# Kernel optimization log

Hardware: AMD Instinct MI355X
Metric: run time of the kernel (lower is better)

The kernel has to match this reference:

```python
import jax, jax.numpy as jnp
import numpy as np

N_NODES = 50000
N_EDGES = 800000
N_GRAPHS = 256
F_IN, HID, EMB = 128, 256, 128
N_GROUPS, N_FAM = 16, 128


def setup_inputs() -> dict:
    key = jax.random.key(0)
    ks = jax.random.split(key, 12)
    x = jax.random.normal(ks[0], (N_NODES, F_IN), dtype=jnp.float32)
    edge_index = jax.random.randint(ks[1], (2, N_EDGES), 0, N_NODES, dtype=jnp.int64)
    batch = jnp.sort(jax.random.randint(ks[2], (N_NODES,), 0, N_GRAPHS, dtype=jnp.int64))
    def lin(k, fi, fo):
        s = 1.0 / np.sqrt(fi)
        return jax.random.uniform(k, (fi, fo), minval=-s, maxval=s, dtype=jnp.float32)
    W1 = lin(ks[3], F_IN, HID); b1 = jnp.zeros((HID,), jnp.float32)
    W2 = lin(ks[4], HID, EMB); b2 = jnp.zeros((EMB,), jnp.float32)
    Wg = lin(ks[5], EMB, N_GROUPS); bg = jnp.zeros((N_GROUPS,), jnp.float32)
    s = 1.0 / np.sqrt(EMB)
    Wf = jax.random.uniform(ks[6], (N_GROUPS, EMB, N_FAM), minval=-s, maxval=s, dtype=jnp.float32)
    bf = jnp.zeros((N_GROUPS, N_FAM), jnp.float32)
    return {"x": x, "edge_index": edge_index, "batch": batch,
            "W1": W1, "b1": b1, "W2": W2, "b2": b2,
            "Wg": Wg, "bg": bg, "Wf": Wf, "bf": bf}


def _gcn_conv(h, src, dst, coef, W, b, n):
    # h: [N, Fin]; src/dst: [E'] (self-loops included); coef: [E'] sym-norm
    hw = h @ W                                    # [N, Fout]
    msg = hw[src] * coef[:, None]                 # gather + scale, [E', Fout]
    out = jax.ops.segment_sum(msg, dst, num_segments=n)  # scatter-add
    return out + b


def reference(x, edge_index, batch, W1, b1, W2, b2, Wg, bg, Wf, bf):
    n = x.shape[0]
    loops = jnp.arange(n, dtype=edge_index.dtype)
    src = jnp.concatenate([edge_index[0], loops])
    dst = jnp.concatenate([edge_index[1], loops])
    # symmetric GCN normalization (deg >= 1 thanks to self-loops)
    deg = jax.ops.segment_sum(jnp.ones_like(dst, dtype=x.dtype), dst, num_segments=n)
    dinv = jax.lax.rsqrt(deg)
    coef = dinv[src] * dinv[dst]

    h1 = jax.nn.relu(_gcn_conv(x, src, dst, coef, W1, b1, n))  # dropout = identity (eval)
    h2 = _gcn_conv(h1, src, dst, coef, W2, b2, n)

    # global mean pool over graphs
    sums = jax.ops.segment_sum(h2, batch, num_segments=N_GRAPHS)
    cnts = jax.ops.segment_sum(jnp.ones((n,), x.dtype), batch, num_segments=N_GRAPHS)
    embeddings = sums / jnp.maximum(cnts, 1.0)[:, None]        # [G, EMB]

    group_logits = embeddings @ Wg + bg                        # [G, n_groups]
    pred_groups = jnp.argmax(group_logits, axis=1)             # routing
    # per-graph routed family classifier (dense equivalent of the dict outputs)
    family_logits = jnp.einsum('gd,gdf->gf', embeddings, Wf[pred_groups]) + bf[pred_groups]
    return embeddings, group_logits, family_logits
```

## Files before the change

kernel.cpp:

```cpp
#include <hip/hip_runtime.h>
#include <hip/hip_fp16.h>
#include <cstddef>
#include <cstdint>

static constexpr int NN   = 50000;
static constexpr int NE   = 800000;
static constexpr int NG   = 256;
static constexpr int FIN  = 128;
static constexpr int HID  = 256;
static constexpr int EMB  = 128;
static constexpr int NGRP = 16;
static constexpr int NFAM = 128;
static constexpr int NETOT = NE + NN;

static constexpr int SCAN_B  = 256;
static constexpr int SCAN_CH = (NN + SCAN_B - 1) / SCAN_B;

using bf16x8 = __attribute__((ext_vector_type(8))) short;
using f32x4  = __attribute__((ext_vector_type(4))) float;

__device__ __forceinline__ unsigned short f2bf(float f) {
    uint32_t u = __float_as_uint(f);
    u += 0x7FFFu + ((u >> 16) & 1u);
    return (unsigned short)(u >> 16);
}
__device__ __forceinline__ float bf2f(unsigned short u) {
    return __uint_as_float((uint32_t)u << 16);
}
__device__ __forceinline__ void unpack_sw(uint32_t v, int& s, float& w) {
    s = (int)(v & 0xFFFFu);
    w = __half2float(__ushort_as_half((unsigned short)(v >> 16)));
}


__global__ void k_count(const int* __restrict__ edst, int* __restrict__ degi, int e) {
    int i = blockIdx.x * blockDim.x + threadIdx.x;
    if (i < e) atomicAdd(degi + edst[i], 1);
}

__global__ void k_prep(const int* __restrict__ degi, const int* __restrict__ batch,
                       float* __restrict__ dinv, int* __restrict__ gstart,
                       float* __restrict__ emb_acc, int n, int G) {
    int i = blockIdx.x * blockDim.x + threadIdx.x;
    if (i < NG * EMB) emb_acc[i] = 0.f;
    if (i >= n) return;
    dinv[i] = rsqrtf((float)(degi[i] + 1));
    int b  = batch[i];
    int pb = (i == 0) ? -1 : batch[i - 1];
    for (int g = pb + 1; g <= b; ++g) gstart[g] = i;
    if (i == n - 1) {
        for (int g = b + 1; g <= G; ++g) gstart[g] = n;
    }
}

__global__ void k_xconv(const float* __restrict__ x, const float* __restrict__ dinv,
                        unsigned short* __restrict__ xs) {
    int t = blockIdx.x * blockDim.x + threadIdx.x;
    size_t i = (size_t)t * 8;
    float dv = dinv[t >> 4];
    float4 a = *(const float4*)(x + i);
    float4 b = *(const float4*)(x + i + 4);
    uint4 o;
    o.x = (uint32_t)f2bf(dv * a.x) | ((uint32_t)f2bf(dv * a.y) << 16);
    o.y = (uint32_t)f2bf(dv * a.z) | ((uint32_t)f2bf(dv * a.w) << 16);
    o.z = (uint32_t)f2bf(dv * b.x) | ((uint32_t)f2bf(dv * b.y) << 16);
    o.w = (uint32_t)f2bf(dv * b.z) | ((uint32_t)f2bf(dv * b.w) << 16);
    *(uint4*)(xs + i) = o;
}

__global__ void k_wconv(const float* __restrict__ W1, const float* __restrict__ W2,
                        unsigned short* __restrict__ W1t, unsigned short* __restrict__ W2t) {
    int t = blockIdx.x * blockDim.x + threadIdx.x;
    if (t < HID * FIN) {
        int nidx = t >> 7, k = t & 127;
        W1t[t] = f2bf(W1[(size_t)k * HID + nidx]);
    } else {
        int u = t - HID * FIN;
        int nidx = u >> 8, k = u & 255;
        W2t[u] = f2bf(W2[(size_t)k * EMB + nidx]);
    }
}


__global__ __launch_bounds__(256) void k_scanA(const int* __restrict__ degi,
                                               const int* __restrict__ gstart,
                                               float* __restrict__ rcnt,
                                               int* __restrict__ row_ptr,
                                               int* __restrict__ bsum, int n) {
    const int b = blockIdx.x, t = threadIdx.x;
    if (b == 0 && t < NG) {
        int c = gstart[t + 1] - gstart[t];
        rcnt[t] = 1.0f / (float)max(c, 1);
    }
    __shared__ int sh[256];
    const int idx = b * SCAN_CH + t;
    int v = 0;
    if (t < SCAN_CH && idx < n) v = degi[idx] + 1;
    sh[t] = v;
    __syncthreads();
    for (int off = 1; off < 256; off <<= 1) {
        int y = (t >= off) ? sh[t - off] : 0;
        __syncthreads();
        if (t >= off) sh[t] += y;
        __syncthreads();
    }
    if (t < SCAN_CH && idx < n) row_ptr[idx] = sh[t] - v;
    if (t == 255) bsum[b] = sh[255];
}

__global__ __launch_bounds__(256) void k_scanB(const int* __restrict__ bsum,
                                               const int* __restrict__ batch,
                                               const float* __restrict__ dinv,
                                               const float* __restrict__ rcnt,
                                               int* __restrict__ row_ptr,
                                               unsigned long long* __restrict__ combo,
                                               uint32_t* __restrict__ eP, int n) {
    __shared__ int sh[SCAN_B];
    const int b = blockIdx.x, t = threadIdx.x;
    sh[t] = bsum[t];
    __syncthreads();
    for (int off = 1; off < SCAN_B; off <<= 1) {
        int y = (t >= off) ? sh[t - off] : 0;
        __syncthreads();
        if (t >= off) sh[t] += y;
        __syncthreads();
    }
    const int boff = (b == 0) ? 0 : sh[b - 1];
    const int idx  = b * SCAN_CH + t;
    if (t < SCAN_CH && idx < n) {
        int rp = row_ptr[idx] + boff;
        row_ptr[idx] = rp;
        unsigned short wh = __half_as_ushort(
            __float2half(dinv[idx] * rcnt[batch[idx]]));
        combo[idx] = ((unsigned long long)wh << 32) | (unsigned int)(rp + 1);
        eP[rp] = (uint32_t)idx | ((uint32_t)wh << 16);
    }
    if (b == 0 && t == 0) row_ptr[n] = sh[SCAN_B - 1];
}


__global__ void k_build(const int* __restrict__ esrc, const int* __restrict__ edst,
                        unsigned long long* __restrict__ combo,
                        uint32_t* __restrict__ eP, int e) {
    int j = blockIdx.x * blockDim.x + threadIdx.x;
    if (j >= e) return;
    int d = edst[j];
    int s = esrc[j];
    unsigned long long old = atomicAdd(combo + d, 1ull);
    uint32_t slot = (uint32_t)old;
    uint32_t wh   = (uint32_t)(old >> 32) & 0xFFFFu;
    eP[slot] = (uint32_t)s | (wh << 16);
}


__global__ __launch_bounds__(256) void k_agg(
        const unsigned short* __restrict__ xs, const int* __restrict__ row_ptr,
        const uint32_t* __restrict__ eP, const float* __restrict__ dinv,
        unsigned short* __restrict__ xa, int n) {
    int node = blockIdx.x * 4 + (threadIdx.x >> 6);
    if (node >= n) return;
    int lane = threadIdx.x & 63;
    int grp = lane >> 4, fl = lane & 15;
    float acc[8] = {};
    int beg = row_ptr[node], end = row_ptr[node + 1];
    for (int j = beg; j < end; j += 4) {
        int jj = j + grp;
        bool valid = jj < end;
        uint32_t ev = __builtin_nontemporal_load(eP + (valid ? jj : beg));
        int s = (int)(ev & 0xFFFFu);
        float m = valid ? 1.f : 0.f;
        bf16x8 v = *(const bf16x8*)(xs + ((size_t)s << 7) + fl * 8);
#pragma unroll
        for (int k = 0; k < 8; ++k)
            acc[k] += m * bf2f((unsigned short)v[k]);
    }
#pragma unroll
    for (int k = 0; k < 8; ++k) {
        acc[k] += __shfl_xor(acc[k], 16);
        acc[k] += __shfl_xor(acc[k], 32);
    }
    if (lane < 16) {
        float di = dinv[node];
        uint4 o;
        o.x = (uint32_t)f2bf(di * acc[0]) | ((uint32_t)f2bf(di * acc[1]) << 16);
        o.y = (uint32_t)f2bf(di * acc[2]) | ((uint32_t)f2bf(di * acc[3]) << 16);
        o.z = (uint32_t)f2bf(di * acc[4]) | ((uint32_t)f2bf(di * acc[5]) << 16);
        o.w = (uint32_t)f2bf(di * acc[6]) | ((uint32_t)f2bf(di * acc[7]) << 16);
        *(uint4*)(xa + ((size_t)node << 7) + fl * 8) = o;
    }
}


__global__ __launch_bounds__(256) void k_fgemm(
        const unsigned short* __restrict__ A,
        const unsigned short* __restrict__ W1t,
        const unsigned short* __restrict__ W2t,
        const float* __restrict__ b1, const float* __restrict__ dinv,
        unsigned short* __restrict__ H, int M) {
    __shared__ unsigned short h1s[64 * 256];
    const int m0 = blockIdx.x * 64;
    const int w  = threadIdx.x >> 6;
    const int l  = threadIdx.x & 63;
    const int lr = l & 15;
    const int lk = l >> 4;

    {
        f32x4 acc[4][4] = {};
        const int n0 = w * 64;
#pragma unroll
        for (int ks = 0; ks < 4; ++ks) {
            const int k0 = ks * 32 + lk * 8;
            bf16x8 bfr[4];
#pragma unroll
            for (int ni = 0; ni < 4; ++ni)
                bfr[ni] = *(const bf16x8*)(W1t + (size_t)(n0 + ni * 16 + lr) * FIN + k0);
#pragma unroll
            for (int mi = 0; mi < 4; ++mi) {
                int row = min(m0 + mi * 16 + lr, M - 1);
                bf16x8 afr = *(const bf16x8*)(A + ((size_t)row << 7) + k0);
#pragma unroll
                for (int ni = 0; ni < 4; ++ni)
                    acc[mi][ni] = __builtin_amdgcn_mfma_f32_16x16x32_bf16(
                        afr, bfr[ni], acc[mi][ni], 0, 0, 0);
            }
        }
#pragma unroll
        for (int ni = 0; ni < 4; ++ni) {
            int col = n0 + ni * 16 + lr;
            float bb = b1[col];
#pragma unroll
            for (int mi = 0; mi < 4; ++mi) {
#pragma unroll
                for (int r = 0; r < 4; ++r) {
                    int rl = mi * 16 + lk * 4 + r;
                    float dv = dinv[min(m0 + rl, M - 1)];
                    float v = fmaxf(acc[mi][ni][r] + bb, 0.f) * dv;
                    int byte = (rl * 512 + col * 2) ^ ((rl & 7) << 4);
                    *(unsigned short*)((char*)h1s + byte) = f2bf(v);
                }
            }
        }
    }
    __syncthreads();
    f32x4 acc2[4][2] = {};
    {
        const int n0 = w * 32;
#pragma unroll
        for (int ks = 0; ks < 8; ++ks) {
            const int k0 = ks * 32 + lk * 8;
            bf16x8 bfr[2];
#pragma unroll
            for (int ni = 0; ni < 2; ++ni)
                bfr[ni] = *(const bf16x8*)(W2t + (size_t)(n0 + ni * 16 + lr) * HID + k0);
#pragma unroll
            for (int mi = 0; mi < 4; ++mi) {
                int rl = mi * 16 + lr;
                int byte = (rl * 512 + k0 * 2) ^ ((rl & 7) << 4);
                bf16x8 afr = *(const bf16x8*)((const char*)h1s + byte);
#pragma unroll
                for (int ni = 0; ni < 2; ++ni)
                    acc2[mi][ni] = __builtin_amdgcn_mfma_f32_16x16x32_bf16(
                        afr, bfr[ni], acc2[mi][ni], 0, 0, 0);
            }
        }
    }
    __syncthreads();
    {
        const int n0 = w * 32;
#pragma unroll
        for (int ni = 0; ni < 2; ++ni) {
            int col = n0 + ni * 16 + lr;
#pragma unroll
            for (int mi = 0; mi < 4; ++mi)
#pragma unroll
                for (int r = 0; r < 4; ++r) {
                    int rl = mi * 16 + lk * 4 + r;
                    h1s[rl * EMB + col] = f2bf(acc2[mi][ni][r]);
                }
        }
    }
    __syncthreads();
    int nrows = min(64, M - m0);
    for (int c = threadIdx.x; c < nrows * 16; c += 256) {
        int rl = c >> 4, cc = c & 15;
        *(uint4*)(H + ((size_t)(m0 + rl) << 7) + cc * 8) =
            *(const uint4*)(h1s + rl * EMB + cc * 8);
    }
}


__global__ __launch_bounds__(256) void k_pool(
        const unsigned short* __restrict__ H, const int* __restrict__ row_ptr,
        const int* __restrict__ gstart, const uint32_t* __restrict__ eP,
        float* __restrict__ emb_acc) {
    __shared__ float red[4][EMB];
    const int g  = blockIdx.x >> 3;
    const int kb = blockIdx.x & 7;
    const int e0 = row_ptr[gstart[g]];
    const int e1 = row_ptr[gstart[g + 1]];
    const int len = e1 - e0;
    const int per = (len + 7) >> 3;
    const int s0  = e0 + kb * per;
    const int s1  = min(s0 + per, e1);
    const int lane = threadIdx.x & 63;
    const int wv   = threadIdx.x >> 6;
    const int grp = lane >> 4, fl = lane & 15;

    float acc[8] = {};
    for (int j = s0 + wv * 4; j < s1; j += 16) {
        int jj = j + grp;
        bool valid = jj < s1;
        uint32_t ev = __builtin_nontemporal_load(eP + (valid ? jj : s0));
        int s; float wgt;
        unpack_sw(ev, s, wgt);
        if (!valid) wgt = 0.f;
        bf16x8 v = *(const bf16x8*)(H + ((size_t)s << 7) + fl * 8);
#pragma unroll
        for (int k = 0; k < 8; ++k)
            acc[k] += wgt * bf2f((unsigned short)v[k]);
    }
#pragma unroll
    for (int k = 0; k < 8; ++k) {
        acc[k] += __shfl_xor(acc[k], 16);
        acc[k] += __shfl_xor(acc[k], 32);
    }
    if (lane < 16) {
#pragma unroll
        for (int k = 0; k < 8; ++k) red[wv][fl * 8 + k] = acc[k];
    }
    __syncthreads();
    int t = threadIdx.x;
    if (t < EMB) {
        float v = red[0][t] + red[1][t] + red[2][t] + red[3][t];
        if (v != 0.f) atomicAdd(&emb_acc[g * EMB + t], v);
    }
}


__global__ __launch_bounds__(128) void k_head(const float* __restrict__ emb_acc,
                                              const int* __restrict__ gstart,
                                              const float* __restrict__ b2,
                                              const float* __restrict__ Wg,
                                              const float* __restrict__ bg,
                                              const float* __restrict__ Wf,
                                              const float* __restrict__ bff,
                                              float* __restrict__ out_emb,
                                              float* __restrict__ out_gl,
                                              float* __restrict__ out_fl) {
    __shared__ float e[EMB];
    __shared__ float gl[NGRP];
    __shared__ int ps;
    int g = blockIdx.x, c = threadIdx.x;
    bool nonempty = gstart[g + 1] > gstart[g];
    float a = emb_acc[g * EMB + c] + (nonempty ? b2[c] : 0.f);
    e[c] = a;
    out_emb[(size_t)g * EMB + c] = a;
    __syncthreads();
    if (c < NGRP) {
        float s = bg[c];
        for (int d = 0; d < EMB; ++d) s += e[d] * Wg[d * NGRP + c];
        gl[c] = s;
        out_gl[g * NGRP + c] = s;
    }
    __syncthreads();
    if (c == 0) {
        int bi = 0;
        float bv = gl[0];
        for (int t2 = 1; t2 < NGRP; ++t2)
            if (gl[t2] > bv) { bv = gl[t2]; bi = t2; }
        ps = bi;
    }
    __syncthreads();
    int pr = ps;
    float s = bff[pr * NFAM + c];
    for (int d = 0; d < EMB; ++d) s += e[d] * Wf[((size_t)pr * EMB + d) * NFAM + c];
    out_fl[g * NFAM + c] = s;
}


extern "C" void kernel_launch(void* const* d_in, const int* in_sizes, int n_in,
                              void* d_out, int out_size, void* d_ws, size_t ws_size,
                              hipStream_t stream) {
    const float* x   = (const float*)d_in[0];
    const int*   ei  = (const int*)d_in[1];
    const int*   bat = (const int*)d_in[2];
    const float* W1  = (const float*)d_in[3];
    const float* b1  = (const float*)d_in[4];
    const float* W2  = (const float*)d_in[5];
    const float* b2  = (const float*)d_in[6];
    const float* Wg  = (const float*)d_in[7];
    const float* bg  = (const float*)d_in[8];
    const float* Wf  = (const float*)d_in[9];
    const float* bf  = (const float*)d_in[10];

    float* out     = (float*)d_out;
    float* out_emb = out;
    float* out_gl  = out + (size_t)NG * EMB;
    float* out_fl  = out_gl + (size_t)NG * NGRP;

    char* w = (char*)d_ws;
    auto alloc = [&](size_t bytes) {
        char* p = w;
        w += (bytes + 255) & ~(size_t)255;
        return p;
    };
    int*                 degi    = (int*)alloc((size_t)NN * 4);
    float*               dinv    = (float*)alloc((size_t)NN * 4);
    int*                 row_ptr = (int*)alloc((size_t)(NN + 1) * 4);
    unsigned long long*  combo   = (unsigned long long*)alloc((size_t)NN * 8);
    int*                 bsum    = (int*)alloc((size_t)SCAN_B * 4);
    uint32_t*            eP      = (uint32_t*)alloc((size_t)NETOT * 4);
    int*                 gstart  = (int*)alloc((size_t)(NG + 1) * 4);
    float*               rcnt    = (float*)alloc((size_t)NG * 4);
    unsigned short*      xs      = (unsigned short*)alloc((size_t)NN * FIN * 2);
    unsigned short*      xa      = (unsigned short*)alloc((size_t)NN * FIN * 2);
    unsigned short*      W1t     = (unsigned short*)alloc((size_t)HID * FIN * 2);
    unsigned short*      W2t     = (unsigned short*)alloc((size_t)EMB * HID * 2);
    unsigned short*      H       = (unsigned short*)alloc((size_t)NN * EMB * 2);
    float*               emb_acc = (float*)alloc((size_t)NG * EMB * 4);

    const int* esrc = ei;
    const int* edst = ei + NE;

    hipMemsetAsync(degi, 0, (size_t)NN * 4, stream);
    k_count<<<(NE + 255) / 256, 256, 0, stream>>>(edst, degi, NE);
    k_prep<<<(NG * HID + 255) / 256, 256, 0, stream>>>(degi, bat, dinv, gstart,
                                                       emb_acc, NN, NG);
    k_xconv<<<(NN * 16) / 256, 256, 0, stream>>>(x, dinv, xs);
    k_wconv<<<(HID * FIN + EMB * HID) / 256, 256, 0, stream>>>(W1, W2, W1t, W2t);
    k_scanA<<<SCAN_B, 256, 0, stream>>>(degi, gstart, rcnt, row_ptr, bsum, NN);
    k_scanB<<<SCAN_B, 256, 0, stream>>>(bsum, bat, dinv, rcnt, row_ptr, combo, eP, NN);
    k_build<<<(NE + 255) / 256, 256, 0, stream>>>(esrc, edst, combo, eP, NE);

    k_agg<<<(NN + 3) / 4, 256, 0, stream>>>(xs, row_ptr, eP, dinv, xa, NN);
    k_fgemm<<<(NN + 63) / 64, 256, 0, stream>>>(xa, W1t, W2t, b1, dinv, H, NN);

    k_pool<<<NG * 8, 256, 0, stream>>>(H, row_ptr, gstart, eP, emb_acc);

    k_head<<<NG, 128, 0, stream>>>(emb_acc, gstart, b2, Wg, bg, Wf, bf,
                                   out_emb, out_gl, out_fl);
}
```

Baseline: 226.7 us.

## Slice CSR build by destination range for atomic locality, pack src/dst edges

```diff
diff --git a/kernel.cpp b/kernel.cpp
--- a/kernel.cpp
+++ b/kernel.cpp
@@ -16,6 +16,10 @@
 static constexpr int SCAN_B  = 256;
 static constexpr int SCAN_CH = (NN + SCAN_B - 1) / SCAN_B;
 
+static constexpr int NSLICE  = 8;
+static constexpr int SLICE_W = (NN + NSLICE - 1) / NSLICE;
+static constexpr int BUILD_RANKS = 64;
+
 using bf16x8 = __attribute__((ext_vector_type(8))) short;
 using f32x4  = __attribute__((ext_vector_type(4))) float;
 
@@ -33,9 +37,15 @@
 }
 
 
-__global__ void k_count(const int* __restrict__ edst, int* __restrict__ degi, int e) {
+__global__ void k_count(const int* __restrict__ esrc, const int* __restrict__ edst,
+                        int* __restrict__ degi, uint32_t* __restrict__ sdpack, int e) {
     int i = blockIdx.x * blockDim.x + threadIdx.x;
-    if (i < e) atomicAdd(degi + edst[i], 1);
+    if (i < e) {
+        int d = edst[i];
+        int s = esrc[i];
+        atomicAdd(degi + d, 1);
+        sdpack[i] = ((uint32_t)d << 16) | (uint32_t)s;
+    }
 }
 
 __global__ void k_prep(const int* __restrict__ degi, const int* __restrict__ batch,
@@ -114,7 +124,7 @@
                                                const float* __restrict__ rcnt,
                                                int* __restrict__ row_ptr,
                                                unsigned long long* __restrict__ combo,
-                                               uint32_t* __restrict__ eP, int n) {
+                                               int n) {
     __shared__ int sh[SCAN_B];
     const int b = blockIdx.x, t = threadIdx.x;
     sh[t] = bsum[t];
@@ -133,23 +143,31 @@
         unsigned short wh = __half_as_ushort(
             __float2half(dinv[idx] * rcnt[batch[idx]]));
         combo[idx] = ((unsigned long long)wh << 32) | (unsigned int)(rp + 1);
-        eP[rp] = (uint32_t)idx | ((uint32_t)wh << 16);
     }
     if (b == 0 && t == 0) row_ptr[n] = sh[SCAN_B - 1];
 }
 
 
-__global__ void k_build(const int* __restrict__ esrc, const int* __restrict__ edst,
-                        unsigned long long* __restrict__ combo,
-                        uint32_t* __restrict__ eP, int e) {
-    int j = blockIdx.x * blockDim.x + threadIdx.x;
-    if (j >= e) return;
-    int d = edst[j];
-    int s = esrc[j];
-    unsigned long long old = atomicAdd(combo + d, 1ull);
-    uint32_t slot = (uint32_t)old;
-    uint32_t wh   = (uint32_t)(old >> 32) & 0xFFFFu;
-    eP[slot] = (uint32_t)s | (wh << 16);
+__global__ __launch_bounds__(256) void k_build(
+        const uint32_t* __restrict__ sdpack, const int* __restrict__ row_ptr,
+        unsigned long long* __restrict__ combo, uint32_t* __restrict__ eP,
+        int n, int e) {
+    const int slice = blockIdx.x & 7;
+    const int rank  = blockIdx.x >> 3;
+    const int lo = slice * SLICE_W;
+    const int hi = min(lo + SLICE_W, n);
+    for (int i = lo + rank * 256 + (int)threadIdx.x; i < hi; i += BUILD_RANKS * 256) {
+        uint32_t rp = (uint32_t)row_ptr[i];
+        uint32_t wh = (uint32_t)(combo[i] >> 32) & 0xFFFFu;
+        eP[rp] = (uint32_t)i | (wh << 16);
+    }
+    for (int j = rank * 256 + (int)threadIdx.x; j < e; j += BUILD_RANKS * 256) {
+        uint32_t p = __builtin_nontemporal_load(sdpack + j);
+        int d = (int)(p >> 16);
+        if (d < lo || d >= hi) continue;
+        unsigned long long old = atomicAdd(combo + d, 1ull);
+        eP[(uint32_t)old] = (p & 0xFFFFu) | (((uint32_t)(old >> 32) & 0xFFFFu) << 16);
+    }
 }
 
 
@@ -409,6 +427,7 @@
     int*                 row_ptr = (int*)alloc((size_t)(NN + 1) * 4);
     unsigned long long*  combo   = (unsigned long long*)alloc((size_t)NN * 8);
     int*                 bsum    = (int*)alloc((size_t)SCAN_B * 4);
+    uint32_t*            sdpack  = (uint32_t*)alloc((size_t)NE * 4);
     uint32_t*            eP      = (uint32_t*)alloc((size_t)NETOT * 4);
     int*                 gstart  = (int*)alloc((size_t)(NG + 1) * 4);
     float*               rcnt    = (float*)alloc((size_t)NG * 4);
@@ -423,14 +442,14 @@
     const int* edst = ei + NE;
 
     hipMemsetAsync(degi, 0, (size_t)NN * 4, stream);
-    k_count<<<(NE + 255) / 256, 256, 0, stream>>>(edst, degi, NE);
+    k_count<<<(NE + 255) / 256, 256, 0, stream>>>(esrc, edst, degi, sdpack, NE);
     k_prep<<<(NG * HID + 255) / 256, 256, 0, stream>>>(degi, bat, dinv, gstart,
                                                        emb_acc, NN, NG);
     k_xconv<<<(NN * 16) / 256, 256, 0, stream>>>(x, dinv, xs);
     k_wconv<<<(HID * FIN + EMB * HID) / 256, 256, 0, stream>>>(W1, W2, W1t, W2t);
     k_scanA<<<SCAN_B, 256, 0, stream>>>(degi, gstart, rcnt, row_ptr, bsum, NN);
-    k_scanB<<<SCAN_B, 256, 0, stream>>>(bsum, bat, dinv, rcnt, row_ptr, combo, eP, NN);
-    k_build<<<(NE + 255) / 256, 256, 0, stream>>>(esrc, edst, combo, eP, NE);
+    k_scanB<<<SCAN_B, 256, 0, stream>>>(bsum, bat, dinv, rcnt, row_ptr, combo, NN);
+    k_build<<<NSLICE * BUILD_RANKS, 256, 0, stream>>>(sdpack, row_ptr, combo, eP, NN, NE);
 
     k_agg<<<(NN + 3) / 4, 256, 0, stream>>>(xs, row_ptr, eP, dinv, xa, NN);
     k_fgemm<<<(NN + 63) / 64, 256, 0, stream>>>(xa, W1t, W2t, b1, dinv, H, NN);
```

After: 226.3 us. About the same (-0.2%).
